# Kernel optimization log

Measured on AMD Instinct MI355X. Metric: run time of the kernel, lower is better.

Reference implementation:

```python
import jax, jax.numpy as jnp
import numpy as np

N_NODES = 50000
N_EDGES = 1200000
F_IN = 128
HID = 64
N_CLASSES = 10
N_GRAPHS = 256
EPS = 1e-5


def setup_inputs() -> dict:
    key = jax.random.key(0)
    ks = jax.random.split(key, 12)
    x = jax.random.normal(ks[0], (N_NODES, F_IN), dtype=jnp.float32)
    edge_index = jax.random.randint(ks[1], (2, N_EDGES), 0, N_NODES, dtype=jnp.int64)
    batch = jnp.sort(jax.random.randint(ks[2], (N_NODES,), 0, N_GRAPHS, dtype=jnp.int64))
    s1 = 1.0 / np.sqrt(F_IN)
    s2 = 1.0 / np.sqrt(HID)
    s3 = 1.0 / np.sqrt(3 * HID)
    return {
        "x": x,
        "edge_index": edge_index,
        "batch": batch,
        "W1": jax.random.normal(ks[3], (F_IN, HID), jnp.float32) * s1,
        "b1": jnp.zeros((HID,), jnp.float32),
        "W2": jax.random.normal(ks[4], (HID, HID), jnp.float32) * s2,  # shared by conv layers 2 and 3
        "b2": jnp.zeros((HID,), jnp.float32),
        "gamma": jnp.ones((HID,), jnp.float32),  # single BatchNorm shared by all 3 layers
        "beta": jnp.zeros((HID,), jnp.float32),
        "lw1": jax.random.normal(ks[5], (3 * HID, HID), jnp.float32) * s3,
        "lb1": jnp.zeros((HID,), jnp.float32),
        "lw2": jax.random.normal(ks[6], (HID, N_CLASSES), jnp.float32) * s2,
        "lb2": jnp.zeros((N_CLASSES,), jnp.float32),
    }


def _batchnorm(h, gamma, beta):
    mu = jnp.mean(h, axis=0)
    var = jnp.mean((h - mu) ** 2, axis=0)  # biased var, training mode
    return (h - mu) * jax.lax.rsqrt(var + EPS) * gamma + beta


def reference(x, edge_index, batch, W1, b1, W2, b2, gamma, beta, lw1, lb1, lw2, lb2):
    src, dst = edge_index[0], edge_index[1]
    # GCN symmetric norm with self-loops: deg includes self-loop weight 1
    deg = jax.ops.segment_sum(jnp.ones((N_EDGES,), x.dtype), dst, num_segments=N_NODES) + 1.0
    dinv = jax.lax.rsqrt(deg)
    coef = dinv[src] * dinv[dst]          # [E]
    self_coef = (dinv * dinv)[:, None]    # [N,1], self-loop contribution

    def gcn_conv(h, W, b):
        h = h @ W
        agg = jax.ops.segment_sum(h[src] * coef[:, None], dst, num_segments=N_NODES)
        return agg + self_coef * h + b

    h = x
    # layer 1 (own weights), layers 2 & 3 share (W2, b2); norm shared across all layers
    h = jax.nn.relu(_batchnorm(gcn_conv(h, W1, b1), gamma, beta))
    h = jax.nn.relu(_batchnorm(gcn_conv(h, W2, b2), gamma, beta))
    h = jax.nn.relu(_batchnorm(gcn_conv(h, W2, b2), gamma, beta))

    # multi-pool: max / mean / add per graph
    pmax = jax.ops.segment_max(h, batch, num_segments=N_GRAPHS)
    pmax = jnp.where(jnp.isfinite(pmax), pmax, 0.0)
    psum = jax.ops.segment_sum(h, batch, num_segments=N_GRAPHS)
    cnt = jax.ops.segment_sum(jnp.ones((N_NODES,), h.dtype), batch, num_segments=N_GRAPHS)
    pmean = psum / jnp.maximum(cnt, 1.0)[:, None]
    emb = jnp.concatenate([pmax, pmean, psum], axis=-1)  # [G, 3H]

    out = jax.nn.relu(emb @ lw1 + lb1) @ lw2 + lb2  # [G, C]
    return out
```

## Files before the change

kernel.cpp:

```cpp
#include <hip/hip_runtime.h>
#include <hip/hip_bf16.h>

#define N_NODES 50000
#define N_EDGES 1200000
#define F_IN 128
#define HID 64
#define N_CLASSES 10
#define N_GRAPHS 256
#define EPSF 1e-5f

__device__ __forceinline__ float bf2f(unsigned short u) {
    return __uint_as_float((unsigned)u << 16);
}
__device__ __forceinline__ unsigned short f2bf(float f) {
    __hip_bfloat16 h = __float2bfloat16(f);
    return *reinterpret_cast<unsigned short*>(&h);
}


__global__ void k_hist(const int* __restrict__ dst, int* __restrict__ cnt) {
    int e = blockIdx.x * blockDim.x + threadIdx.x;
    if (e < N_EDGES) atomicAdd(&cnt[dst[e]], 1);
}

__global__ __launch_bounds__(1024) void k_scan(const int* __restrict__ cnt,
                                               int* __restrict__ offs,
                                               int* __restrict__ cursor,
                                               float* __restrict__ dinv) {
    __shared__ int wsum[16];
    __shared__ int s_carry;
    int tid = threadIdx.x;
    int lane = tid & 63, wid = tid >> 6;
    if (tid == 0) s_carry = 0;
    __syncthreads();
    for (int base = 0; base < N_NODES; base += 1024) {
        int i = base + tid;
        int v = (i < N_NODES) ? cnt[i] : 0;
        if (i < N_NODES) dinv[i] = rsqrtf((float)v + 1.0f);
        int x = v;
        #pragma unroll
        for (int d = 1; d < 64; d <<= 1) {
            int y = __shfl_up(x, (unsigned)d);
            if (lane >= d) x += y;
        }
        if (lane == 63) wsum[wid] = x;
        __syncthreads();
        if (tid == 0) {
            int run = 0;
            for (int w = 0; w < 16; ++w) { int t = wsum[w]; wsum[w] = run; run += t; }
        }
        __syncthreads();
        int carry = s_carry;
        int excl = carry + wsum[wid] + (x - v);
        if (i < N_NODES) { offs[i] = excl; cursor[i] = excl; }
        __syncthreads();
        if (tid == 1023) s_carry = carry + wsum[15] + x;
        __syncthreads();
    }
    if (tid == 0) offs[N_NODES] = s_carry;
}

__global__ void k_fill(const int* __restrict__ esrc, const int* __restrict__ edst,
                       const float* __restrict__ dinv,
                       int* __restrict__ cursor, unsigned int* __restrict__ csr) {
    int e = blockIdx.x * blockDim.x + threadIdx.x;
    if (e < N_EDGES) {
        int d = edst[e];
        int s = esrc[e];
        int pos = atomicAdd(&cursor[d], 1);
        csr[pos] = ((unsigned)f2bf(dinv[s]) << 16) | (unsigned)s;
    }
}

__global__ void k_bounds(const int* __restrict__ batch, int* __restrict__ gstart) {
    int v = blockIdx.x * blockDim.x + threadIdx.x;
    if (v >= N_NODES) return;
    if (v == 0) {
        int b = batch[0];
        for (int g = 0; g <= b; ++g) gstart[g] = 0;
    } else {
        int b0 = batch[v - 1], b1 = batch[v];
        for (int g = b0 + 1; g <= b1; ++g) gstart[g] = v;
    }
    if (v == N_NODES - 1) {
        int b = batch[v];
        for (int g = b + 1; g <= N_GRAPHS; ++g) gstart[g] = N_NODES;
    }
}


template <int K, bool NORM>
__global__ __launch_bounds__(256, 2) void k_gemm(const float* __restrict__ A,
                                                 const float* __restrict__ W,
                                                 unsigned short* __restrict__ out_bf,
                                                 const float* __restrict__ stats,
                                                 const float* __restrict__ gamma,
                                                 const float* __restrict__ beta) {
    __shared__ float sW[K * 64];
    __shared__ float sA[32][68];
    __shared__ float ssc[128];
    __shared__ float ssh[128];
    int tid = threadIdx.x;
    for (int i = tid; i < K * 16; i += 256) ((float4*)sW)[i] = ((const float4*)W)[i];
    if (NORM && tid < K) {
        const float invN = 1.0f / (float)N_NODES;
        float mu = stats[tid] * invN;
        float var = stats[64 + tid] * invN - mu * mu;
        float sc = rsqrtf(var + EPSF) * gamma[tid];
        ssc[tid] = sc;
        ssh[tid] = beta[tid] - mu * sc;
    }
    __syncthreads();

    int row0 = blockIdx.x * 64;
    int c0 = (tid & 15) * 4;
    int r0 = (tid >> 4) * 4;
    float acc[4][4] = {};

    #pragma unroll 1
    for (int k0 = 0; k0 < K; k0 += 32) {
        #pragma unroll
        for (int i = 0; i < 2; ++i) {
            int idx = tid + i * 256;
            int row = idx >> 3;
            int kq = idx & 7;
            int grow = row0 + row;
            float4 v = make_float4(0.f, 0.f, 0.f, 0.f);
            if (grow < N_NODES) v = *(const float4*)&A[(size_t)grow * K + k0 + kq * 4];
            if (NORM) {
                int kb = k0 + kq * 4;
                v.x = fmaxf(v.x * ssc[kb + 0] + ssh[kb + 0], 0.f);
                v.y = fmaxf(v.y * ssc[kb + 1] + ssh[kb + 1], 0.f);
                v.z = fmaxf(v.z * ssc[kb + 2] + ssh[kb + 2], 0.f);
                v.w = fmaxf(v.w * ssc[kb + 3] + ssh[kb + 3], 0.f);
            }
            sA[kq * 4 + 0][row] = v.x;
            sA[kq * 4 + 1][row] = v.y;
            sA[kq * 4 + 2][row] = v.z;
            sA[kq * 4 + 3][row] = v.w;
        }
        __syncthreads();
        #pragma unroll 4
        for (int k = 0; k < 32; ++k) {
            float4 a = *(const float4*)&sA[k][r0];
            float4 w = *(const float4*)&sW[(k0 + k) * 64 + c0];
            acc[0][0] += a.x * w.x; acc[0][1] += a.x * w.y; acc[0][2] += a.x * w.z; acc[0][3] += a.x * w.w;
            acc[1][0] += a.y * w.x; acc[1][1] += a.y * w.y; acc[1][2] += a.y * w.z; acc[1][3] += a.y * w.w;
            acc[2][0] += a.z * w.x; acc[2][1] += a.z * w.y; acc[2][2] += a.z * w.z; acc[2][3] += a.z * w.w;
            acc[3][0] += a.w * w.x; acc[3][1] += a.w * w.y; acc[3][2] += a.w * w.z; acc[3][3] += a.w * w.w;
        }
        __syncthreads();
    }
    #pragma unroll
    for (int i = 0; i < 4; ++i) {
        int row = row0 + r0 + i;
        if (row < N_NODES) {
            ushort4 o;
            o.x = f2bf(acc[i][0]); o.y = f2bf(acc[i][1]);
            o.z = f2bf(acc[i][2]); o.w = f2bf(acc[i][3]);
            *(ushort4*)&out_bf[(size_t)row * 64 + c0] = o;
        }
    }
}

__global__ __launch_bounds__(256) void k_agg(const unsigned short* __restrict__ hw,
                                             const int* __restrict__ offs,
                                             const unsigned int* __restrict__ csr,
                                             const float* __restrict__ dinv,
                                             const float* __restrict__ bias,
                                             float* __restrict__ hpre,
                                             float* __restrict__ stats) {
    __shared__ float sred[128];
    if (threadIdx.x < 128) sred[threadIdx.x] = 0.f;
    __syncthreads();
    int lane = threadIdx.x & 63;
    int wave = blockIdx.x * 4 + (threadIdx.x >> 6);
    int nw = gridDim.x * 4;
    float b = bias[lane];
    float lsum = 0.f, lsq = 0.f;
    for (int v = wave; v < N_NODES; v += nw) {
        float dv = dinv[v];
        int s = offs[v], e = offs[v + 1];
        float inner = dv * bf2f(hw[(size_t)v * 64 + lane]);
        int j = s;
        for (; j + 16 <= e; j += 16) {
            unsigned int q[16];
            #pragma unroll
            for (int t = 0; t < 16; ++t) q[t] = csr[j + t];
            float hh[16];
            #pragma unroll
            for (int t = 0; t < 16; ++t)
                hh[t] = bf2f(hw[(size_t)(q[t] & 0xFFFFu) * 64 + lane]);
            #pragma unroll
            for (int t = 0; t < 16; ++t)
                inner += bf2f((unsigned short)(q[t] >> 16)) * hh[t];
        }
        for (; j + 4 <= e; j += 4) {
            unsigned int q0 = csr[j], q1 = csr[j + 1], q2 = csr[j + 2], q3 = csr[j + 3];
            float h0 = bf2f(hw[(size_t)(q0 & 0xFFFFu) * 64 + lane]);
            float h1 = bf2f(hw[(size_t)(q1 & 0xFFFFu) * 64 + lane]);
            float h2 = bf2f(hw[(size_t)(q2 & 0xFFFFu) * 64 + lane]);
            float h3 = bf2f(hw[(size_t)(q3 & 0xFFFFu) * 64 + lane]);
            inner += bf2f((unsigned short)(q0 >> 16)) * h0;
            inner += bf2f((unsigned short)(q1 >> 16)) * h1;
            inner += bf2f((unsigned short)(q2 >> 16)) * h2;
            inner += bf2f((unsigned short)(q3 >> 16)) * h3;
        }
        for (; j < e; ++j) {
            unsigned int q = csr[j];
            inner += bf2f((unsigned short)(q >> 16)) * bf2f(hw[(size_t)(q & 0xFFFFu) * 64 + lane]);
        }
        float acc = dv * inner + b;
        hpre[(size_t)v * 64 + lane] = acc;
        lsum += acc;
        lsq += acc * acc;
    }
    atomicAdd(&sred[lane], lsum);
    atomicAdd(&sred[64 + lane], lsq);
    __syncthreads();
    if (threadIdx.x < 128) atomicAdd(&stats[threadIdx.x], sred[threadIdx.x]);
}

__global__ __launch_bounds__(256) void k_pool(const float* __restrict__ hpre,
                                              const float* __restrict__ stats,
                                              const float* __restrict__ gamma,
                                              const float* __restrict__ beta,
                                              const int* __restrict__ gstart,
                                              const float* __restrict__ lw1,
                                              const float* __restrict__ lb1,
                                              const float* __restrict__ lw2,
                                              const float* __restrict__ lb2,
                                              float* __restrict__ out) {
    __shared__ float smax[4][64];
    __shared__ float ssum[4][64];
    __shared__ float emb[192];
    __shared__ float hid[64];
    int g = blockIdx.x;
    int lane = threadIdx.x & 63;
    int wid = threadIdx.x >> 6;
    int s = gstart[g], e = gstart[g + 1];

    const float invN = 1.0f / (float)N_NODES;
    float mu = stats[lane] * invN;
    float var = stats[64 + lane] * invN - mu * mu;
    float sc = rsqrtf(var + EPSF) * gamma[lane];
    float sh = beta[lane] - mu * sc;

    float mx = 0.f, sm = 0.f;
    for (int v = s + wid; v < e; v += 4) {
        float h = fmaxf(hpre[(size_t)v * 64 + lane] * sc + sh, 0.f);
        mx = fmaxf(mx, h);
        sm += h;
    }
    smax[wid][lane] = mx;
    ssum[wid][lane] = sm;
    __syncthreads();
    if (wid == 0) {
        float m = fmaxf(fmaxf(smax[0][lane], smax[1][lane]), fmaxf(smax[2][lane], smax[3][lane]));
        float su = ssum[0][lane] + ssum[1][lane] + ssum[2][lane] + ssum[3][lane];
        float inv = 1.0f / fmaxf((float)(e - s), 1.0f);
        emb[lane] = m;
        emb[64 + lane] = su * inv;
        emb[128 + lane] = su;
    }
    __syncthreads();
    if (wid == 0) {
        float acc = lb1[lane];
        #pragma unroll 4
        for (int k = 0; k < 192; ++k) acc += emb[k] * lw1[k * 64 + lane];
        hid[lane] = fmaxf(acc, 0.f);
    }
    __syncthreads();
    if (threadIdx.x < N_CLASSES) {
        int j = threadIdx.x;
        float o = lb2[j];
        #pragma unroll 8
        for (int k = 0; k < 64; ++k) o += hid[k] * lw2[k * 10 + j];
        out[(size_t)g * 10 + j] = o;
    }
}


extern "C" void kernel_launch(void* const* d_in, const int* in_sizes, int n_in,
                              void* d_out, int out_size, void* d_ws, size_t ws_size,
                              hipStream_t stream) {
    const float* x     = (const float*)d_in[0];
    const int* eidx    = (const int*)d_in[1];
    const int* batch   = (const int*)d_in[2];
    const float* W1    = (const float*)d_in[3];
    const float* b1    = (const float*)d_in[4];
    const float* W2    = (const float*)d_in[5];
    const float* b2    = (const float*)d_in[6];
    const float* gamma = (const float*)d_in[7];
    const float* beta  = (const float*)d_in[8];
    const float* lw1   = (const float*)d_in[9];
    const float* lb1   = (const float*)d_in[10];
    const float* lw2   = (const float*)d_in[11];
    const float* lb2   = (const float*)d_in[12];
    float* out = (float*)d_out;

    const int* e_src = eidx;
    const int* e_dst = eidx + N_EDGES;

    char* p = (char*)d_ws;
    auto carve = [&](size_t bytes) { char* r = p; p += (bytes + 255) & ~(size_t)255; return r; };
    int*   cnt   = (int*)carve((size_t)N_NODES * 4);
    float* stats = (float*)carve(3 * 128 * 4);
    size_t zero_bytes = (size_t)(p - (char*)d_ws);
    int*   offs   = (int*)carve((size_t)(N_NODES + 1) * 4);
    int*   cursor = (int*)carve((size_t)N_NODES * 4);
    float* dinv   = (float*)carve((size_t)N_NODES * 4);
    int*   gstart = (int*)carve((size_t)(N_GRAPHS + 1) * 4);
    unsigned int* csr = (unsigned int*)carve((size_t)N_EDGES * 4);
    unsigned short* B0 = (unsigned short*)carve((size_t)N_NODES * 64 * 2);
    float* B1     = (float*)carve((size_t)N_NODES * 64 * 4);

    hipMemsetAsync(d_ws, 0, zero_bytes, stream);

    k_hist<<<(N_EDGES + 255) / 256, 256, 0, stream>>>(e_dst, cnt);
    k_scan<<<1, 1024, 0, stream>>>(cnt, offs, cursor, dinv);
    k_fill<<<(N_EDGES + 255) / 256, 256, 0, stream>>>(e_src, e_dst, dinv, cursor, csr);
    k_bounds<<<(N_NODES + 255) / 256, 256, 0, stream>>>(batch, gstart);

    const int GEMM_GRID = (N_NODES + 63) / 64;
    k_gemm<128, false><<<GEMM_GRID, 256, 0, stream>>>(x, W1, B0, nullptr, nullptr, nullptr);
    k_agg<<<2048, 256, 0, stream>>>(B0, offs, csr, dinv, b1, B1, stats);
    k_gemm<64, true><<<GEMM_GRID, 256, 0, stream>>>(B1, W2, B0, stats, gamma, beta);
    k_agg<<<2048, 256, 0, stream>>>(B0, offs, csr, dinv, b2, B1, stats + 128);
    k_gemm<64, true><<<GEMM_GRID, 256, 0, stream>>>(B1, W2, B0, stats + 128, gamma, beta);
    k_agg<<<2048, 256, 0, stream>>>(B0, offs, csr, dinv, b2, B1, stats + 256);
    k_pool<<<N_GRAPHS, 256, 0, stream>>>(B1, stats + 256, gamma, beta, gstart,
                                         lw1, lb1, lw2, lb2, out);
}
```

Measured before the change: 570.3 us.

## Replace per-node CSR fill with coarse destination binning and LDS-atomic aggregation

```diff
diff --git a/kernel.cpp b/kernel.cpp
--- a/kernel.cpp
+++ b/kernel.cpp
@@ -9,6 +9,10 @@
 #define N_GRAPHS 256
 #define EPSF 1e-5f
 
+#define BSZ 128
+#define NB 391
+#define BIN_CHUNK 8192
+
 __device__ __forceinline__ float bf2f(unsigned short u) {
     return __uint_as_float((unsigned)u << 16);
 }
@@ -25,7 +29,7 @@
 
 __global__ __launch_bounds__(1024) void k_scan(const int* __restrict__ cnt,
                                                int* __restrict__ offs,
-                                               int* __restrict__ cursor,
+                                               int* __restrict__ bcur,
                                                float* __restrict__ dinv) {
     __shared__ int wsum[16];
     __shared__ int s_carry;
@@ -52,23 +56,51 @@
         __syncthreads();
         int carry = s_carry;
         int excl = carry + wsum[wid] + (x - v);
-        if (i < N_NODES) { offs[i] = excl; cursor[i] = excl; }
+        if (i < N_NODES) offs[i] = excl;
         __syncthreads();
         if (tid == 1023) s_carry = carry + wsum[15] + x;
         __syncthreads();
     }
     if (tid == 0) offs[N_NODES] = s_carry;
-}
-
-__global__ void k_fill(const int* __restrict__ esrc, const int* __restrict__ edst,
-                       const float* __restrict__ dinv,
-                       int* __restrict__ cursor, unsigned int* __restrict__ csr) {
-    int e = blockIdx.x * blockDim.x + threadIdx.x;
-    if (e < N_EDGES) {
-        int d = edst[e];
-        int s = esrc[e];
-        int pos = atomicAdd(&cursor[d], 1);
-        csr[pos] = ((unsigned)f2bf(dinv[s]) << 16) | (unsigned)s;
+    __syncthreads();
+    for (int b = tid; b < NB; b += 1024) bcur[b] = offs[b * BSZ];
+}
+
+__global__ __launch_bounds__(256) void k_bin(const int* __restrict__ esrc,
+                                             const int* __restrict__ edst,
+                                             const float* __restrict__ dinv,
+                                             int* __restrict__ bcur,
+                                             uint2* __restrict__ binned) {
+    __shared__ int lcnt[NB];
+    __shared__ int lbase[NB];
+    int tid = threadIdx.x;
+    for (int i = tid; i < NB; i += 256) lcnt[i] = 0;
+    __syncthreads();
+    int e0 = blockIdx.x * BIN_CHUNK;
+    int myidx[32];
+    #pragma unroll
+    for (int t = 0; t < 32; ++t) {
+        int i = e0 + t * 256 + tid;
+        if (i < N_EDGES) {
+            int b = edst[i] >> 7;
+            int idx = atomicAdd(&lcnt[b], 1);
+            myidx[t] = (b << 16) | idx;
+        }
+    }
+    __syncthreads();
+    for (int b = tid; b < NB; b += 256)
+        if (lcnt[b]) lbase[b] = atomicAdd(&bcur[b], lcnt[b]);
+    __syncthreads();
+    #pragma unroll
+    for (int t = 0; t < 32; ++t) {
+        int i = e0 + t * 256 + tid;
+        if (i < N_EDGES) {
+            int m = myidx[t];
+            int b = m >> 16, idx = m & 0xFFFF;
+            int s = esrc[i], d = edst[i];
+            binned[lbase[b] + idx] =
+                make_uint2(((unsigned)d << 16) | (unsigned)s, __float_as_int(dinv[s]));
+        }
     }
 }
 
@@ -163,62 +195,64 @@
     }
 }
 
-__global__ __launch_bounds__(256) void k_agg(const unsigned short* __restrict__ hw,
-                                             const int* __restrict__ offs,
-                                             const unsigned int* __restrict__ csr,
-                                             const float* __restrict__ dinv,
-                                             const float* __restrict__ bias,
-                                             float* __restrict__ hpre,
-                                             float* __restrict__ stats) {
+__global__ __launch_bounds__(1024) void k_aggb(const unsigned short* __restrict__ hw,
+                                               const int* __restrict__ offs,
+                                               const uint2* __restrict__ binned,
+                                               const float* __restrict__ dinv,
+                                               const float* __restrict__ bias,
+                                               float* __restrict__ hpre,
+                                               float* __restrict__ stats) {
+    __shared__ float acc[BSZ * 64];
     __shared__ float sred[128];
-    if (threadIdx.x < 128) sred[threadIdx.x] = 0.f;
-    __syncthreads();
-    int lane = threadIdx.x & 63;
-    int wave = blockIdx.x * 4 + (threadIdx.x >> 6);
-    int nw = gridDim.x * 4;
+    int tid = threadIdx.x;
+    int lane = tid & 63;
+    int wid = tid >> 6;
+    int v0 = blockIdx.x * BSZ;
+    int v1 = min(v0 + BSZ, N_NODES);
+    int nn = v1 - v0;
+
+    #pragma unroll
+    for (int i = 0; i < 8; ++i) ((float4*)acc)[tid + i * 1024] = make_float4(0.f, 0.f, 0.f, 0.f);
+    if (tid < 128) sred[tid] = 0.f;
+    __syncthreads();
+
+    int estart = offs[v0];
+    int eend = offs[v1];
+
+    for (int base = estart + wid * 64; base < eend; base += 1024) {
+        unsigned ex = 0, ey = 0;
+        if (base + lane < eend) {
+            uint2 E = binned[base + lane];
+            ex = E.x; ey = E.y;
+        }
+        int nt = min(64, eend - base);
+        #pragma unroll 4
+        for (int t = 0; t < nt; ++t) {
+            unsigned px = (unsigned)__builtin_amdgcn_readlane((int)ex, t);
+            float w = __uint_as_float((unsigned)__builtin_amdgcn_readlane((int)ey, t));
+            int src = (int)(px & 0xFFFFu);
+            int lv = (int)(px >> 16) - v0;
+            float h = bf2f(hw[(size_t)src * 64 + lane]);
+            atomicAdd(&acc[lv * 64 + lane], w * h);
+        }
+    }
+    __syncthreads();
+
     float b = bias[lane];
     float lsum = 0.f, lsq = 0.f;
-    for (int v = wave; v < N_NODES; v += nw) {
+    for (int lv = wid; lv < nn; lv += 16) {
+        int v = v0 + lv;
         float dv = dinv[v];
-        int s = offs[v], e = offs[v + 1];
-        float inner = dv * bf2f(hw[(size_t)v * 64 + lane]);
-        int j = s;
-        for (; j + 16 <= e; j += 16) {
-            unsigned int q[16];
-            #pragma unroll
-            for (int t = 0; t < 16; ++t) q[t] = csr[j + t];
-            float hh[16];
-            #pragma unroll
-            for (int t = 0; t < 16; ++t)
-                hh[t] = bf2f(hw[(size_t)(q[t] & 0xFFFFu) * 64 + lane]);
-            #pragma unroll
-            for (int t = 0; t < 16; ++t)
-                inner += bf2f((unsigned short)(q[t] >> 16)) * hh[t];
-        }
-        for (; j + 4 <= e; j += 4) {
-            unsigned int q0 = csr[j], q1 = csr[j + 1], q2 = csr[j + 2], q3 = csr[j + 3];
-            float h0 = bf2f(hw[(size_t)(q0 & 0xFFFFu) * 64 + lane]);
-            float h1 = bf2f(hw[(size_t)(q1 & 0xFFFFu) * 64 + lane]);
-            float h2 = bf2f(hw[(size_t)(q2 & 0xFFFFu) * 64 + lane]);
-            float h3 = bf2f(hw[(size_t)(q3 & 0xFFFFu) * 64 + lane]);
-            inner += bf2f((unsigned short)(q0 >> 16)) * h0;
-            inner += bf2f((unsigned short)(q1 >> 16)) * h1;
-            inner += bf2f((unsigned short)(q2 >> 16)) * h2;
-            inner += bf2f((unsigned short)(q3 >> 16)) * h3;
-        }
-        for (; j < e; ++j) {
-            unsigned int q = csr[j];
-            inner += bf2f((unsigned short)(q >> 16)) * bf2f(hw[(size_t)(q & 0xFFFFu) * 64 + lane]);
-        }
-        float acc = dv * inner + b;
-        hpre[(size_t)v * 64 + lane] = acc;
-        lsum += acc;
-        lsq += acc * acc;
+        float hv = bf2f(hw[(size_t)v * 64 + lane]);
+        float a = dv * acc[lv * 64 + lane] + dv * dv * hv + b;
+        hpre[(size_t)v * 64 + lane] = a;
+        lsum += a;
+        lsq += a * a;
     }
     atomicAdd(&sred[lane], lsum);
     atomicAdd(&sred[64 + lane], lsq);
     __syncthreads();
-    if (threadIdx.x < 128) atomicAdd(&stats[threadIdx.x], sred[threadIdx.x]);
+    if (tid < 128) atomicAdd(&stats[tid], sred[tid]);
 }
 
 __global__ __launch_bounds__(256) void k_pool(const float* __restrict__ hpre,
@@ -308,27 +342,27 @@
     float* stats = (float*)carve(3 * 128 * 4);
     size_t zero_bytes = (size_t)(p - (char*)d_ws);
     int*   offs   = (int*)carve((size_t)(N_NODES + 1) * 4);
-    int*   cursor = (int*)carve((size_t)N_NODES * 4);
+    int*   bcur   = (int*)carve((size_t)NB * 4);
     float* dinv   = (float*)carve((size_t)N_NODES * 4);
     int*   gstart = (int*)carve((size_t)(N_GRAPHS + 1) * 4);
-    unsigned int* csr = (unsigned int*)carve((size_t)N_EDGES * 4);
+    uint2* binned = (uint2*)carve((size_t)N_EDGES * 8);
     unsigned short* B0 = (unsigned short*)carve((size_t)N_NODES * 64 * 2);
     float* B1     = (float*)carve((size_t)N_NODES * 64 * 4);
 
     hipMemsetAsync(d_ws, 0, zero_bytes, stream);
 
     k_hist<<<(N_EDGES + 255) / 256, 256, 0, stream>>>(e_dst, cnt);
-    k_scan<<<1, 1024, 0, stream>>>(cnt, offs, cursor, dinv);
-    k_fill<<<(N_EDGES + 255) / 256, 256, 0, stream>>>(e_src, e_dst, dinv, cursor, csr);
+    k_scan<<<1, 1024, 0, stream>>>(cnt, offs, bcur, dinv);
+    k_bin<<<(N_EDGES + BIN_CHUNK - 1) / BIN_CHUNK, 256, 0, stream>>>(e_src, e_dst, dinv, bcur, binned);
     k_bounds<<<(N_NODES + 255) / 256, 256, 0, stream>>>(batch, gstart);
 
     const int GEMM_GRID = (N_NODES + 63) / 64;
     k_gemm<128, false><<<GEMM_GRID, 256, 0, stream>>>(x, W1, B0, nullptr, nullptr, nullptr);
-    k_agg<<<2048, 256, 0, stream>>>(B0, offs, csr, dinv, b1, B1, stats);
+    k_aggb<<<NB, 1024, 0, stream>>>(B0, offs, binned, dinv, b1, B1, stats);
     k_gemm<64, true><<<GEMM_GRID, 256, 0, stream>>>(B1, W2, B0, stats, gamma, beta);
-    k_agg<<<2048, 256, 0, stream>>>(B0, offs, csr, dinv, b2, B1, stats + 128);
+    k_aggb<<<NB, 1024, 0, stream>>>(B0, offs, binned, dinv, b2, B1, stats + 128);
     k_gemm<64, true><<<GEMM_GRID, 256, 0, stream>>>(B1, W2, B0, stats + 128, gamma, beta);
-    k_agg<<<2048, 256, 0, stream>>>(B0, offs, csr, dinv, b2, B1, stats + 256);
+    k_aggb<<<NB, 1024, 0, stream>>>(B0, offs, binned, dinv, b2, B1, stats + 256);
     k_pool<<<N_GRAPHS, 256, 0, stream>>>(B1, stats + 256, gamma, beta, gstart,
                                          lw1, lb1, lw2, lb2, out);
 }
```

Result: slower. 1.884 ms (+230.3%).

## Build CSR via two-pass bucketed binning instead of global atomic scatter

Applied to the files above, without the earlier changes.

```diff
diff --git a/kernel.cpp b/kernel.cpp
--- a/kernel.cpp
+++ b/kernel.cpp
@@ -9,6 +9,10 @@
 #define N_GRAPHS 256
 #define EPSF 1e-5f
 
+#define BSZ 128
+#define NB 391
+#define BIN_CHUNK 8192
+
 __device__ __forceinline__ float bf2f(unsigned short u) {
     return __uint_as_float((unsigned)u << 16);
 }
@@ -25,7 +29,7 @@
 
 __global__ __launch_bounds__(1024) void k_scan(const int* __restrict__ cnt,
                                                int* __restrict__ offs,
-                                               int* __restrict__ cursor,
+                                               int* __restrict__ bcur,
                                                float* __restrict__ dinv) {
     __shared__ int wsum[16];
     __shared__ int s_carry;
@@ -52,23 +56,71 @@
         __syncthreads();
         int carry = s_carry;
         int excl = carry + wsum[wid] + (x - v);
-        if (i < N_NODES) { offs[i] = excl; cursor[i] = excl; }
+        if (i < N_NODES) offs[i] = excl;
         __syncthreads();
         if (tid == 1023) s_carry = carry + wsum[15] + x;
         __syncthreads();
     }
     if (tid == 0) offs[N_NODES] = s_carry;
-}
-
-__global__ void k_fill(const int* __restrict__ esrc, const int* __restrict__ edst,
-                       const float* __restrict__ dinv,
-                       int* __restrict__ cursor, unsigned int* __restrict__ csr) {
-    int e = blockIdx.x * blockDim.x + threadIdx.x;
-    if (e < N_EDGES) {
-        int d = edst[e];
-        int s = esrc[e];
-        int pos = atomicAdd(&cursor[d], 1);
-        csr[pos] = ((unsigned)f2bf(dinv[s]) << 16) | (unsigned)s;
+    __syncthreads();
+    for (int b = tid; b < NB; b += 1024) bcur[b] = offs[b * BSZ];
+}
+
+__global__ __launch_bounds__(256) void k_bin(const int* __restrict__ esrc,
+                                             const int* __restrict__ edst,
+                                             const float* __restrict__ dinv,
+                                             int* __restrict__ bcur,
+                                             uint2* __restrict__ binned) {
+    __shared__ int lcnt[NB];
+    __shared__ int lbase[NB];
+    int tid = threadIdx.x;
+    for (int i = tid; i < NB; i += 256) lcnt[i] = 0;
+    __syncthreads();
+    int e0 = blockIdx.x * BIN_CHUNK;
+    int myidx[32];
+    #pragma unroll
+    for (int t = 0; t < 32; ++t) {
+        int i = e0 + t * 256 + tid;
+        if (i < N_EDGES) {
+            int b = edst[i] >> 7;
+            int idx = atomicAdd(&lcnt[b], 1);
+            myidx[t] = (b << 16) | idx;
+        }
+    }
+    __syncthreads();
+    for (int b = tid; b < NB; b += 256)
+        if (lcnt[b]) lbase[b] = atomicAdd(&bcur[b], lcnt[b]);
+    __syncthreads();
+    #pragma unroll
+    for (int t = 0; t < 32; ++t) {
+        int i = e0 + t * 256 + tid;
+        if (i < N_EDGES) {
+            int m = myidx[t];
+            int b = m >> 16, idx = m & 0xFFFF;
+            int s = esrc[i], d = edst[i];
+            binned[lbase[b] + idx] =
+                make_uint2(((unsigned)d << 16) | (unsigned)s, __float_as_int(dinv[s]));
+        }
+    }
+}
+
+__global__ __launch_bounds__(256) void k_fill2(const uint2* __restrict__ binned,
+                                               const int* __restrict__ offs,
+                                               unsigned int* __restrict__ csr) {
+    __shared__ int cur[BSZ];
+    int v0 = blockIdx.x * BSZ;
+    int v1 = min(v0 + BSZ, N_NODES);
+    int tid = threadIdx.x;
+    for (int i = tid; i < BSZ; i += 256)
+        cur[i] = (v0 + i < N_NODES) ? offs[v0 + i] : 0;
+    __syncthreads();
+    int s = offs[v0], e = offs[v1];
+    for (int j = s + tid; j < e; j += 256) {
+        uint2 E = binned[j];
+        int lv = (int)(E.x >> 16) - v0;
+        unsigned src = E.x & 0xFFFFu;
+        int pos = atomicAdd(&cur[lv], 1);
+        csr[pos] = ((unsigned)f2bf(__uint_as_float(E.y)) << 16) | src;
     }
 }
 
@@ -308,9 +360,10 @@
     float* stats = (float*)carve(3 * 128 * 4);
     size_t zero_bytes = (size_t)(p - (char*)d_ws);
     int*   offs   = (int*)carve((size_t)(N_NODES + 1) * 4);
-    int*   cursor = (int*)carve((size_t)N_NODES * 4);
+    int*   bcur   = (int*)carve((size_t)NB * 4);
     float* dinv   = (float*)carve((size_t)N_NODES * 4);
     int*   gstart = (int*)carve((size_t)(N_GRAPHS + 1) * 4);
+    uint2* binned = (uint2*)carve((size_t)N_EDGES * 8);
     unsigned int* csr = (unsigned int*)carve((size_t)N_EDGES * 4);
     unsigned short* B0 = (unsigned short*)carve((size_t)N_NODES * 64 * 2);
     float* B1     = (float*)carve((size_t)N_NODES * 64 * 4);
@@ -318,8 +371,9 @@
     hipMemsetAsync(d_ws, 0, zero_bytes, stream);
 
     k_hist<<<(N_EDGES + 255) / 256, 256, 0, stream>>>(e_dst, cnt);
-    k_scan<<<1, 1024, 0, stream>>>(cnt, offs, cursor, dinv);
-    k_fill<<<(N_EDGES + 255) / 256, 256, 0, stream>>>(e_src, e_dst, dinv, cursor, csr);
+    k_scan<<<1, 1024, 0, stream>>>(cnt, offs, bcur, dinv);
+    k_bin<<<(N_EDGES + BIN_CHUNK - 1) / BIN_CHUNK, 256, 0, stream>>>(e_src, e_dst, dinv, bcur, binned);
+    k_fill2<<<NB, 256, 0, stream>>>(binned, offs, csr);
     k_bounds<<<(N_NODES + 255) / 256, 256, 0, stream>>>(batch, gstart);
 
     const int GEMM_GRID = (N_NODES + 63) / 64;
```

Measured after the change: 534.2 us. 1.07x faster.
